# Optimization experiments

Measured on AMD Instinct MI355X. Metric: run time of the kernel, lower is better.

## Reference

```python
import jax, jax.numpy as jnp
import numpy as np

N = 100000
E = 1600000
IN_CH, HID_CH, OUT_CH, HEADS = 128, 32, 64, 4
NEG_SLOPE = 0.2


def gat_conv(x, src, dst, W, att_src, att_dst, bias, concat):
    """PyG-style GATConv (inference; dropout off). src/dst include self-loops.
    x: [N, Fin], W: [Fin, H*C], att_*: [H, C], bias: [H*C] or [C]."""
    n = x.shape[0]
    H, C = att_src.shape
    h = (x @ W).reshape(n, H, C)                      # [N, H, C]
    a_s = jnp.sum(h * att_src, axis=-1)               # [N, H]
    a_d = jnp.sum(h * att_dst, axis=-1)               # [N, H]
    e = jax.nn.leaky_relu(a_s[src] + a_d[dst], NEG_SLOPE)   # [E, H]
    # segment softmax over incoming edges of each dst node
    e_max = jax.ops.segment_max(e, dst, num_segments=n)     # [N, H]
    e_exp = jnp.exp(e - e_max[dst])                          # [E, H]
    denom = jax.ops.segment_sum(e_exp, dst, num_segments=n) # [N, H]
    alpha = e_exp / (denom[dst] + 1e-16)                     # [E, H]
    msg = h[src] * alpha[:, :, None]                         # [E, H, C]
    out = jax.ops.segment_sum(msg, dst, num_segments=n)     # [N, H, C]
    out = out.reshape(n, H * C) if concat else out.mean(axis=1)
    return out + bias


def setup_inputs() -> dict:
    key = jax.random.key(0)
    ks = jax.random.split(key, 10)
    g = 1.0 / np.sqrt(IN_CH)
    g2 = 1.0 / np.sqrt(HID_CH * HEADS)
    return {
        "x": jax.random.normal(ks[0], (N, IN_CH), dtype=jnp.float32),
        "edge_index": jax.random.randint(ks[1], (2, E), 0, N, dtype=jnp.int64),
        "W1": jax.random.normal(ks[2], (IN_CH, HEADS * HID_CH), dtype=jnp.float32) * g,
        "att_src1": jax.random.normal(ks[3], (HEADS, HID_CH), dtype=jnp.float32) * g,
        "att_dst1": jax.random.normal(ks[4], (HEADS, HID_CH), dtype=jnp.float32) * g,
        "b1": jnp.zeros((HEADS * HID_CH,), dtype=jnp.float32),
        "W2": jax.random.normal(ks[5], (HEADS * HID_CH, OUT_CH), dtype=jnp.float32) * g2,
        "att_src2": jax.random.normal(ks[6], (1, OUT_CH), dtype=jnp.float32) * g2,
        "att_dst2": jax.random.normal(ks[7], (1, OUT_CH), dtype=jnp.float32) * g2,
        "b2": jnp.zeros((OUT_CH,), dtype=jnp.float32),
    }


def reference(x, edge_index, W1, att_src1, att_dst1, b1, W2, att_src2, att_dst2, b2):
    n = x.shape[0]
    # GATConv adds self-loops by default (fixed-size concat: jit friendly)
    loops = jnp.arange(n, dtype=edge_index.dtype)
    src = jnp.concatenate([edge_index[0], loops])
    dst = jnp.concatenate([edge_index[1], loops])
    h = gat_conv(x, src, dst, W1, att_src1, att_dst1, b1, concat=True)
    h = jax.nn.elu(h)
    return gat_conv(h, src, dst, W2, att_src2, att_dst2, b2, concat=False)
```

## Files before the change

kernel.cpp:

```cpp
#include <hip/hip_runtime.h>
#include <hip/hip_fp16.h>

#define NEG_SLOPE 0.2f
#define BKN 128
#define MAXNB 1024
#define GRP 256
#define LOG2E 1.44269504f

typedef _Float16 half_t;
typedef __attribute__((ext_vector_type(2))) _Float16 half2v;
typedef __attribute__((ext_vector_type(4))) _Float16 half4;
typedef __attribute__((ext_vector_type(8))) _Float16 half8;
typedef __attribute__((ext_vector_type(4))) float floatx4;

#if __has_builtin(__builtin_amdgcn_fdot2)
#define FDOT2(a, b, c) __builtin_amdgcn_fdot2((a), (b), (c), false)
#else
#define FDOT2(a, b, c) ((float)(a)[0] * (float)(b)[0] + (float)(a)[1] * (float)(b)[1] + (c))
#endif

__global__ __launch_bounds__(256) void w_convert2(
    const float* __restrict__ W1, half_t* __restrict__ Wt1,
    const float* __restrict__ W2, half_t* __restrict__ Wt2)
{
    int i = blockIdx.x * 256 + threadIdx.x;
    if (i < 128 * 128) {
        int k = i / 128, nn = i % 128;
        Wt1[nn * 128 + k] = (half_t)W1[i];
    } else if (i < 128 * 128 + 128 * 64) {
        int j = i - 128 * 128;
        int k = j / 64, nn = j % 64;
        Wt2[nn * 128 + k] = (half_t)W2[j];
    }
}

template<int BN, int HEADS, bool INHALF>
__global__ __launch_bounds__(256) void gemm_mfma(
    const void* __restrict__ Xv, const half_t* __restrict__ Wt,
    const float* __restrict__ atts, const float* __restrict__ attd,
    half_t* __restrict__ H, float* __restrict__ As, float* __restrict__ Ad,
    int n)
{
    constexpr int K  = 128;
    constexpr int NT = BN / 16;
    constexpr int TPH = NT / HEADS;

    __shared__ half_t Wl[BN * K];
    __shared__ half_t Xl[64 * K];

    const int t = threadIdx.x;
    const int wave = t >> 6, lane = t & 63;
    const int quad = lane >> 4, c = lane & 15;

    float att_s[NT], att_d[NT];
    #pragma unroll
    for (int nt = 0; nt < NT; ++nt) {
        att_s[nt] = atts[nt * 16 + c] * LOG2E;
        att_d[nt] = attd[nt * 16 + c] * LOG2E;
    }

    for (int i = t; i < BN * 16; i += 256) {
        int row = i >> 4, cid = i & 15;
        half8 v = *(const half8*)(Wt + row * K + cid * 8);
        *(half8*)(Wl + row * K + ((cid ^ (row & 15)) << 3)) = v;
    }

    const int numTiles = (n + 63) / 64;
    for (int tile = blockIdx.x; tile < numTiles; tile += gridDim.x) {
        const int row0 = tile * 64;
        __syncthreads();
        for (int i = t; i < 1024; i += 256) {
            int m = i >> 4, cid = i & 15;
            int row = row0 + m;
            half8 h;
            #pragma unroll
            for (int z = 0; z < 8; ++z) h[z] = (half_t)0.f;
            if (row < n) {
                if constexpr (INHALF) {
                    h = *(const half8*)((const half_t*)Xv + (size_t)row * K + cid * 8);
                } else {
                    const float4* src = (const float4*)((const float*)Xv + (size_t)row * K + cid * 8);
                    float4 a = src[0], b = src[1];
                    h[0]=(half_t)a.x; h[1]=(half_t)a.y; h[2]=(half_t)a.z; h[3]=(half_t)a.w;
                    h[4]=(half_t)b.x; h[5]=(half_t)b.y; h[6]=(half_t)b.z; h[7]=(half_t)b.w;
                }
            }
            *(half8*)(Xl + m * K + ((cid ^ (m & 15)) << 3)) = h;
        }
        __syncthreads();

        floatx4 acc[NT];
        #pragma unroll
        for (int i = 0; i < NT; ++i) acc[i] = (floatx4)(0.f);

        #pragma unroll
        for (int kc = 0; kc < 4; ++kc) {
            int cid = kc * 4 + quad;
            half8 afrag = *(const half8*)(Xl + (wave * 16 + c) * K + ((cid ^ c) << 3));
            #pragma unroll
            for (int nt = 0; nt < NT; ++nt) {
                half8 bfrag = *(const half8*)(Wl + (nt * 16 + c) * K + ((cid ^ c) << 3));
                acc[nt] = __builtin_amdgcn_mfma_f32_16x16x32_f16(afrag, bfrag, acc[nt], 0, 0, 0);
            }
        }

        #pragma unroll
        for (int reg = 0; reg < 4; ++reg) {
            int row = row0 + wave * 16 + quad * 4 + reg;
            bool ok = row < n;
            if (ok) {
                #pragma unroll
                for (int nt = 0; nt < NT; ++nt)
                    H[(size_t)row * BN + nt * 16 + c] = (half_t)acc[nt][reg];
            }
            #pragma unroll
            for (int h = 0; h < HEADS; ++h) {
                float ps = 0.f, pd = 0.f;
                #pragma unroll
                for (int u = 0; u < TPH; ++u) {
                    int nt = h * TPH + u;
                    ps += acc[nt][reg] * att_s[nt];
                    pd += acc[nt][reg] * att_d[nt];
                }
                #pragma unroll
                for (int off = 1; off < 16; off <<= 1) {
                    ps += __shfl_xor(ps, off);
                    pd += __shfl_xor(pd, off);
                }
                if (ok && c == 0) {
                    As[(size_t)row * HEADS + h] = ps;
                    Ad[(size_t)row * HEADS + h] = pd;
                }
            }
        }
    }
}

__global__ __launch_bounds__(256) void ghist(
    const int* __restrict__ ei, int E, int Etot, int NB, int chunk,
    int* __restrict__ cnt)
{
    __shared__ int h[MAXNB];
    int g = blockIdx.x;
    for (int i = threadIdx.x; i < NB; i += 256) h[i] = 0;
    __syncthreads();
    int lo = g * chunk, hi = min(Etot, lo + chunk);
    for (int e = lo + threadIdx.x; e < hi; e += 256) {
        int dst = (e < E) ? ei[E + e] : (e - E);
        atomicAdd(&h[dst >> 7], 1);
    }
    __syncthreads();
    for (int i = threadIdx.x; i < NB; i += 256) cnt[i * GRP + g] = h[i];
}

__global__ __launch_bounds__(256) void scan_blocks(
    int* __restrict__ data, int n, int* __restrict__ bsum)
{
    __shared__ int s[256];
    int t = threadIdx.x;
    int idx = blockIdx.x * 1024 + t * 4;
    int4 v = make_int4(0, 0, 0, 0);
    if (idx + 3 < n)      v = *(const int4*)(data + idx);
    else {
        if (idx     < n) v.x = data[idx];
        if (idx + 1 < n) v.y = data[idx+1];
        if (idx + 2 < n) v.z = data[idx+2];
        if (idx + 3 < n) v.w = data[idx+3];
    }
    int tsum = v.x + v.y + v.z + v.w;
    s[t] = tsum;
    __syncthreads();
    for (int off = 1; off < 256; off <<= 1) {
        int x = (t >= off) ? s[t - off] : 0;
        __syncthreads();
        s[t] += x;
        __syncthreads();
    }
    int excl = s[t] - tsum;
    if (t == 255) bsum[blockIdx.x] = s[255];
    if (idx     < n) data[idx]     = excl;
    if (idx + 1 < n) data[idx + 1] = excl + v.x;
    if (idx + 2 < n) data[idx + 2] = excl + v.x + v.y;
    if (idx + 3 < n) data[idx + 3] = excl + v.x + v.y + v.z;
}

__global__ __launch_bounds__(256) void scan_sums(int* __restrict__ bsum, int nb)
{
    __shared__ int s[256];
    int t = threadIdx.x;
    int v = (t < nb) ? bsum[t] : 0;
    s[t] = v;
    __syncthreads();
    for (int off = 1; off < 256; off <<= 1) {
        int x = (t >= off) ? s[t - off] : 0;
        __syncthreads();
        s[t] += x;
        __syncthreads();
    }
    if (t < nb) bsum[t] = s[t] - v;
}

__global__ __launch_bounds__(256) void pass1_scatter(
    const int* __restrict__ ei, int E, int Etot, int NB, int chunk,
    const int* __restrict__ S, const int* __restrict__ bsum,
    unsigned* __restrict__ tmp)
{
    __shared__ int cur[MAXNB];
    int g = blockIdx.x;
    for (int i = threadIdx.x; i < NB; i += 256) {
        int idx = i * GRP + g;
        cur[i] = S[idx] + bsum[idx >> 10];
    }
    __syncthreads();
    int lo = g * chunk, hi = min(Etot, lo + chunk);
    for (int e = lo + threadIdx.x; e < hi; e += 256) {
        int src, dst;
        if (e < E) { src = ei[e]; dst = ei[E + e]; }
        else       { src = dst = e - E; }
        int pos = atomicAdd(&cur[dst >> 7], 1);
        tmp[pos] = ((unsigned)src << 7) | (unsigned)(dst & (BKN - 1));
    }
}

__global__ __launch_bounds__(256) void pass2_sort(
    const unsigned* __restrict__ tmp, const int* __restrict__ S,
    const int* __restrict__ bsum, int NB, int Etot,
    int* __restrict__ offs, int* __restrict__ esrc, int n)
{
    __shared__ int cnt[BKN];
    __shared__ int sc[BKN];
    __shared__ int cur[BKN];
    int bk = blockIdx.x;
    int t  = threadIdx.x;
    if (t < BKN) cnt[t] = 0;
    __syncthreads();
    int lo = S[bk * GRP] + bsum[(bk * GRP) >> 10];
    int hi = (bk + 1 < NB) ? (S[(bk + 1) * GRP] + bsum[((bk + 1) * GRP) >> 10]) : Etot;
    for (int i = lo + t; i < hi; i += 256)
        atomicAdd(&cnt[tmp[i] & (BKN - 1)], 1);
    __syncthreads();
    int v = (t < BKN) ? cnt[t] : 0;
    if (t < BKN) sc[t] = v;
    __syncthreads();
    for (int off = 1; off < BKN; off <<= 1) {
        int x = (t < BKN && t >= off) ? sc[t - off] : 0;
        __syncthreads();
        if (t < BKN) sc[t] += x;
        __syncthreads();
    }
    if (t < BKN) {
        int node = bk * BKN + t;
        if (node < n) offs[node] = lo + sc[t];
        cur[t] = lo + sc[t] - v;
    }
    __syncthreads();
    for (int i = lo + t; i < hi; i += 256) {
        unsigned w = tmp[i];
        int p = atomicAdd(&cur[w & (BKN - 1)], 1);
        esrc[p] = (int)(w >> 7);
    }
}

__global__ __launch_bounds__(256) void agg1(
    const int* __restrict__ offs, const int* __restrict__ esrc,
    const half8* __restrict__ H8, const float* __restrict__ As,
    const float* __restrict__ Ad, const float* __restrict__ bias,
    half_t* __restrict__ X2h, int n)
{
    int v    = (blockIdx.x * 256 + threadIdx.x) >> 6;
    int lane = threadIdx.x & 63;
    if (v >= n) return;
    int q    = lane >> 4;
    int li   = lane & 15;
    int head = li >> 2;
    int end = offs[v];
    int beg = v ? offs[v - 1] : 0;
    float adv = Ad[(size_t)v * 4 + head];
    half2v one; one[0] = (half_t)1.f; one[1] = (half_t)1.f;
    float a[8];
    #pragma unroll
    for (int f = 0; f < 8; ++f) a[f] = 0.f;
    float den = 0.f;
    int j = beg + q;
    for (; j + 12 < end; j += 16) {
        int s0 = esrc[j], s1 = esrc[j + 4], s2 = esrc[j + 8], s3 = esrc[j + 12];
        float e0 = As[(unsigned)(s0 * 4 + head)] + adv;
        float e1 = As[(unsigned)(s1 * 4 + head)] + adv;
        float e2 = As[(unsigned)(s2 * 4 + head)] + adv;
        float e3 = As[(unsigned)(s3 * 4 + head)] + adv;
        half8 q0 = H8[(unsigned)(s0 * 16 + li)];
        half8 q1 = H8[(unsigned)(s1 * 16 + li)];
        half8 q2 = H8[(unsigned)(s2 * 16 + li)];
        half8 q3 = H8[(unsigned)(s3 * 16 + li)];
        float w0 = __builtin_amdgcn_exp2f(fmaxf(e0, NEG_SLOPE * e0));
        float w1 = __builtin_amdgcn_exp2f(fmaxf(e1, NEG_SLOPE * e1));
        float w2 = __builtin_amdgcn_exp2f(fmaxf(e2, NEG_SLOPE * e2));
        float w3 = __builtin_amdgcn_exp2f(fmaxf(e3, NEG_SLOPE * e3));
        half2v wp01; wp01[0] = (half_t)w0; wp01[1] = (half_t)w1;
        half2v wp23; wp23[0] = (half_t)w2; wp23[1] = (half_t)w3;
        #pragma unroll
        for (int f = 0; f < 8; ++f) {
            half2v p01; p01[0] = q0[f]; p01[1] = q1[f];
            half2v p23; p23[0] = q2[f]; p23[1] = q3[f];
            a[f] = FDOT2(p01, wp01, a[f]);
            a[f] = FDOT2(p23, wp23, a[f]);
        }
        den = FDOT2(wp01, one, den);
        den = FDOT2(wp23, one, den);
    }
    for (; j + 4 < end; j += 8) {
        int s0 = esrc[j], s1 = esrc[j + 4];
        float e0 = As[(unsigned)(s0 * 4 + head)] + adv;
        float e1 = As[(unsigned)(s1 * 4 + head)] + adv;
        half8 q0 = H8[(unsigned)(s0 * 16 + li)];
        half8 q1 = H8[(unsigned)(s1 * 16 + li)];
        float w0 = __builtin_amdgcn_exp2f(fmaxf(e0, NEG_SLOPE * e0));
        float w1 = __builtin_amdgcn_exp2f(fmaxf(e1, NEG_SLOPE * e1));
        half2v wp; wp[0] = (half_t)w0; wp[1] = (half_t)w1;
        #pragma unroll
        for (int f = 0; f < 8; ++f) {
            half2v p; p[0] = q0[f]; p[1] = q1[f];
            a[f] = FDOT2(p, wp, a[f]);
        }
        den = FDOT2(wp, one, den);
    }
    for (; j < end; j += 4) {
        int s = esrc[j];
        float e = As[(unsigned)(s * 4 + head)] + adv;
        half8 q0 = H8[(unsigned)(s * 16 + li)];
        float w = __builtin_amdgcn_exp2f(fmaxf(e, NEG_SLOPE * e));
        #pragma unroll
        for (int f = 0; f < 8; ++f) a[f] += w * (float)q0[f];
        den += w;
    }
    #pragma unroll
    for (int f = 0; f < 8; ++f) {
        a[f] += __shfl_xor(a[f], 16);
        a[f] += __shfl_xor(a[f], 32);
    }
    den += __shfl_xor(den, 16);
    den += __shfl_xor(den, 32);
    if (q == 0) {
        float inv = 1.f / (den + 1e-16f);
        float4 b0 = ((const float4*)bias)[2 * li];
        float4 b1 = ((const float4*)bias)[2 * li + 1];
        float o[8];
        o[0] = a[0] * inv + b0.x; o[1] = a[1] * inv + b0.y;
        o[2] = a[2] * inv + b0.z; o[3] = a[3] * inv + b0.w;
        o[4] = a[4] * inv + b1.x; o[5] = a[5] * inv + b1.y;
        o[6] = a[6] * inv + b1.z; o[7] = a[7] * inv + b1.w;
        half8 h;
        #pragma unroll
        for (int f = 0; f < 8; ++f) {
            float e = o[f] > 0.f ? o[f] : __expf(o[f]) - 1.f;
            h[f] = (half_t)e;
        }
        *(half8*)(X2h + (size_t)v * 128 + li * 8) = h;
    }
}

__global__ __launch_bounds__(256) void agg2(
    const int* __restrict__ offs, const int* __restrict__ esrc,
    const half8* __restrict__ H8, const float* __restrict__ As,
    const float* __restrict__ Ad, const float* __restrict__ bias,
    float* __restrict__ out, int n)
{
    int v    = (blockIdx.x * 256 + threadIdx.x) >> 6;
    int lane = threadIdx.x & 63;
    if (v >= n) return;
    int g  = lane >> 3;
    int li = lane & 7;
    int end = offs[v];
    int beg = v ? offs[v - 1] : 0;
    float adv = Ad[v];
    half2v one; one[0] = (half_t)1.f; one[1] = (half_t)1.f;
    float a[8];
    #pragma unroll
    for (int f = 0; f < 8; ++f) a[f] = 0.f;
    float den = 0.f;
    int j = beg + g;
    for (; j + 24 < end; j += 32) {
        int s0 = esrc[j], s1 = esrc[j + 8], s2 = esrc[j + 16], s3 = esrc[j + 24];
        float e0 = As[s0] + adv;
        float e1 = As[s1] + adv;
        float e2 = As[s2] + adv;
        float e3 = As[s3] + adv;
        half8 q0 = H8[(unsigned)(s0 * 8 + li)];
        half8 q1 = H8[(unsigned)(s1 * 8 + li)];
        half8 q2 = H8[(unsigned)(s2 * 8 + li)];
        half8 q3 = H8[(unsigned)(s3 * 8 + li)];
        float w0 = __builtin_amdgcn_exp2f(fmaxf(e0, NEG_SLOPE * e0));
        float w1 = __builtin_amdgcn_exp2f(fmaxf(e1, NEG_SLOPE * e1));
        float w2 = __builtin_amdgcn_exp2f(fmaxf(e2, NEG_SLOPE * e2));
        float w3 = __builtin_amdgcn_exp2f(fmaxf(e3, NEG_SLOPE * e3));
        half2v wp01; wp01[0] = (half_t)w0; wp01[1] = (half_t)w1;
        half2v wp23; wp23[0] = (half_t)w2; wp23[1] = (half_t)w3;
        #pragma unroll
        for (int f = 0; f < 8; ++f) {
            half2v p01; p01[0] = q0[f]; p01[1] = q1[f];
            half2v p23; p23[0] = q2[f]; p23[1] = q3[f];
            a[f] = FDOT2(p01, wp01, a[f]);
            a[f] = FDOT2(p23, wp23, a[f]);
        }
        den = FDOT2(wp01, one, den);
        den = FDOT2(wp23, one, den);
    }
    for (; j + 8 < end; j += 16) {
        int s0 = esrc[j], s1 = esrc[j + 8];
        float e0 = As[s0] + adv;
        float e1 = As[s1] + adv;
        half8 q0 = H8[(unsigned)(s0 * 8 + li)];
        half8 q1 = H8[(unsigned)(s1 * 8 + li)];
        float w0 = __builtin_amdgcn_exp2f(fmaxf(e0, NEG_SLOPE * e0));
        float w1 = __builtin_amdgcn_exp2f(fmaxf(e1, NEG_SLOPE * e1));
        half2v wp; wp[0] = (half_t)w0; wp[1] = (half_t)w1;
        #pragma unroll
        for (int f = 0; f < 8; ++f) {
            half2v p; p[0] = q0[f]; p[1] = q1[f];
            a[f] = FDOT2(p, wp, a[f]);
        }
        den = FDOT2(wp, one, den);
    }
    for (; j < end; j += 8) {
        int s = esrc[j];
        float e = As[s] + adv;
        half8 q0 = H8[(unsigned)(s * 8 + li)];
        float w = __builtin_amdgcn_exp2f(fmaxf(e, NEG_SLOPE * e));
        #pragma unroll
        for (int f = 0; f < 8; ++f) a[f] += w * (float)q0[f];
        den += w;
    }
    #pragma unroll
    for (int f = 0; f < 8; ++f) {
        a[f] += __shfl_xor(a[f], 8);
        a[f] += __shfl_xor(a[f], 16);
        a[f] += __shfl_xor(a[f], 32);
    }
    den += __shfl_xor(den, 8);
    den += __shfl_xor(den, 16);
    den += __shfl_xor(den, 32);
    if (lane < 8) {
        float inv = 1.f / (den + 1e-16f);
        float4 b0 = ((const float4*)bias)[2 * li];
        float4 b1 = ((const float4*)bias)[2 * li + 1];
        float4* o4 = (float4*)(out + (size_t)v * 64);
        o4[2 * li]     = make_float4(a[0] * inv + b0.x, a[1] * inv + b0.y,
                                     a[2] * inv + b0.z, a[3] * inv + b0.w);
        o4[2 * li + 1] = make_float4(a[4] * inv + b1.x, a[5] * inv + b1.y,
                                     a[6] * inv + b1.z, a[7] * inv + b1.w);
    }
}

extern "C" void kernel_launch(void* const* d_in, const int* in_sizes, int n_in,
                              void* d_out, int out_size, void* d_ws, size_t ws_size,
                              hipStream_t stream)
{
    (void)n_in; (void)out_size; (void)ws_size;
    const float* x   = (const float*)d_in[0];
    const int*   ei  = (const int*)  d_in[1];
    const float* W1  = (const float*)d_in[2];
    const float* as1 = (const float*)d_in[3];
    const float* ad1 = (const float*)d_in[4];
    const float* b1  = (const float*)d_in[5];
    const float* W2  = (const float*)d_in[6];
    const float* as2 = (const float*)d_in[7];
    const float* ad2 = (const float*)d_in[8];
    const float* b2  = (const float*)d_in[9];
    float* out = (float*)d_out;

    const int n    = in_sizes[0] / 128;
    const int E    = in_sizes[1] / 2;
    const int Etot = E + n;
    const int NB   = (n + BKN - 1) / BKN;
    const int chunk = (Etot + GRP - 1) / GRP;

    char* p = (char*)d_ws;
    half_t* Hh  = (half_t*)p; p += (size_t)n * 128 * sizeof(half_t);
    half_t* X2h = (half_t*)p; p += (size_t)n * 128 * sizeof(half_t);
    float* As1 = (float*)p;   p += (size_t)n * 4 * sizeof(float);
    float* Ad1 = (float*)p;   p += (size_t)n * 4 * sizeof(float);
    int* offs  = (int*)p;     p += (size_t)n * sizeof(int);
    int* esrc  = (int*)p;     p += (size_t)Etot * sizeof(int);
    unsigned* tmp = (unsigned*)p; p += (size_t)Etot * sizeof(unsigned);
    int* cnt   = (int*)p;     p += (size_t)NB * GRP * sizeof(int);
    int* bsum  = (int*)p;     p += 1024;
    half_t* Wt1 = (half_t*)p; p += 128 * 128 * sizeof(half_t);
    half_t* Wt2 = (half_t*)p; p += 64 * 128 * sizeof(half_t);

    const int scan_n  = NB * GRP;
    const int scan_nb = (scan_n + 1023) / 1024;

    w_convert2<<<(128 * 192 + 255) / 256, 256, 0, stream>>>(W1, Wt1, W2, Wt2);

    ghist<<<GRP, 256, 0, stream>>>(ei, E, Etot, NB, chunk, cnt);
    scan_blocks<<<scan_nb, 256, 0, stream>>>(cnt, scan_n, bsum);
    scan_sums<<<1, 256, 0, stream>>>(bsum, scan_nb);
    pass1_scatter<<<GRP, 256, 0, stream>>>(ei, E, Etot, NB, chunk, cnt, bsum, tmp);
    pass2_sort<<<NB, 256, 0, stream>>>(tmp, cnt, bsum, NB, Etot, offs, esrc, n);

    const int gtiles = (n + 63) / 64;

    gemm_mfma<128, 4, false><<<gtiles, 256, 0, stream>>>(x, Wt1, as1, ad1, Hh, As1, Ad1, n);
    agg1<<<(n * 64 + 255) / 256, 256, 0, stream>>>(offs, esrc, (const half8*)Hh, As1, Ad1, b1, X2h, n);

    gemm_mfma<64, 1, true><<<gtiles, 256, 0, stream>>>(X2h, Wt2, as2, ad2, Hh, As1, Ad1, n);
    agg2<<<(n * 64 + 255) / 256, 256, 0, stream>>>(offs, esrc, (const half8*)Hh, As1, Ad1, b2, out, n);
}
```

Before: 320.7 us.

## Replace two-pass bucket sort CSR build with per-node atomic counting sort

Replaces the bucketed histogram, scatter and per-bucket local sort with a per-node degree histogram using global atomics, a scan over node degrees, and a single scatter pass that writes source indices directly through per-node atomic cursors. Weight conversion is folded into the histogram kernel, and block sums are added lazily in the aggregation kernels. This removes one full pass over the edges and the temporary packed buffer, at the cost of contended global atomics and non-deterministic edge order within each node.

```diff
diff --git a/kernel.cpp b/kernel.cpp
--- a/kernel.cpp
+++ b/kernel.cpp
@@ -2,9 +2,6 @@
 #include <hip/hip_fp16.h>
 
 #define NEG_SLOPE 0.2f
-#define BKN 128
-#define MAXNB 1024
-#define GRP 256
 #define LOG2E 1.44269504f
 
 typedef _Float16 half_t;
@@ -18,21 +15,6 @@
 #else
 #define FDOT2(a, b, c) ((float)(a)[0] * (float)(b)[0] + (float)(a)[1] * (float)(b)[1] + (c))
 #endif
-
-__global__ __launch_bounds__(256) void w_convert2(
-    const float* __restrict__ W1, half_t* __restrict__ Wt1,
-    const float* __restrict__ W2, half_t* __restrict__ Wt2)
-{
-    int i = blockIdx.x * 256 + threadIdx.x;
-    if (i < 128 * 128) {
-        int k = i / 128, nn = i % 128;
-        Wt1[nn * 128 + k] = (half_t)W1[i];
-    } else if (i < 128 * 128 + 128 * 64) {
-        int j = i - 128 * 128;
-        int k = j / 64, nn = j % 64;
-        Wt2[nn * 128 + k] = (half_t)W2[j];
-    }
-}
 
 template<int BN, int HEADS, bool INHALF>
 __global__ __launch_bounds__(256) void gemm_mfma(
@@ -136,36 +118,41 @@
     }
 }
 
-__global__ __launch_bounds__(256) void ghist(
-    const int* __restrict__ ei, int E, int Etot, int NB, int chunk,
-    int* __restrict__ cnt)
-{
-    __shared__ int h[MAXNB];
-    int g = blockIdx.x;
-    for (int i = threadIdx.x; i < NB; i += 256) h[i] = 0;
-    __syncthreads();
-    int lo = g * chunk, hi = min(Etot, lo + chunk);
-    for (int e = lo + threadIdx.x; e < hi; e += 256) {
+__global__ __launch_bounds__(256) void ghist_g(
+    const int* __restrict__ ei, int E, int Etot, int* __restrict__ deg,
+    const float* __restrict__ W1, half_t* __restrict__ Wt1,
+    const float* __restrict__ W2, half_t* __restrict__ Wt2)
+{
+    int iw = blockIdx.x * 256 + threadIdx.x;
+    if (iw < 128 * 128) {
+        int k = iw / 128, nn = iw % 128;
+        Wt1[nn * 128 + k] = (half_t)W1[iw];
+    } else if (iw < 128 * 128 + 128 * 64) {
+        int jx = iw - 128 * 128;
+        int k = jx / 64, nn = jx % 64;
+        Wt2[nn * 128 + k] = (half_t)W2[jx];
+    }
+    int stride = gridDim.x * 256;
+    for (int e = blockIdx.x * 256 + threadIdx.x; e < Etot; e += stride) {
         int dst = (e < E) ? ei[E + e] : (e - E);
-        atomicAdd(&h[dst >> 7], 1);
-    }
-    __syncthreads();
-    for (int i = threadIdx.x; i < NB; i += 256) cnt[i * GRP + g] = h[i];
-}
-
-__global__ __launch_bounds__(256) void scan_blocks(
-    int* __restrict__ data, int n, int* __restrict__ bsum)
+        atomicAdd(&deg[dst], 1);
+    }
+}
+
+__global__ __launch_bounds__(256) void scan_blocks_dc(
+    const int* __restrict__ deg, int n, int* __restrict__ offs,
+    int* __restrict__ cur, int* __restrict__ bsum)
 {
     __shared__ int s[256];
     int t = threadIdx.x;
     int idx = blockIdx.x * 1024 + t * 4;
     int4 v = make_int4(0, 0, 0, 0);
-    if (idx + 3 < n)      v = *(const int4*)(data + idx);
+    if (idx + 3 < n)      v = *(const int4*)(deg + idx);
     else {
-        if (idx     < n) v.x = data[idx];
-        if (idx + 1 < n) v.y = data[idx+1];
-        if (idx + 2 < n) v.z = data[idx+2];
-        if (idx + 3 < n) v.w = data[idx+3];
+        if (idx     < n) v.x = deg[idx];
+        if (idx + 1 < n) v.y = deg[idx+1];
+        if (idx + 2 < n) v.z = deg[idx+2];
+        if (idx + 3 < n) v.w = deg[idx+3];
     }
     int tsum = v.x + v.y + v.z + v.w;
     s[t] = tsum;
@@ -178,10 +165,11 @@
     }
     int excl = s[t] - tsum;
     if (t == 255) bsum[blockIdx.x] = s[255];
-    if (idx     < n) data[idx]     = excl;
-    if (idx + 1 < n) data[idx + 1] = excl + v.x;
-    if (idx + 2 < n) data[idx + 2] = excl + v.x + v.y;
-    if (idx + 3 < n) data[idx + 3] = excl + v.x + v.y + v.z;
+    int p0 = excl, p1 = p0 + v.x, p2 = p1 + v.y, p3 = p2 + v.z;
+    if (idx     < n) { cur[idx]     = p0; offs[idx]     = p1; }
+    if (idx + 1 < n) { cur[idx + 1] = p1; offs[idx + 1] = p2; }
+    if (idx + 2 < n) { cur[idx + 2] = p2; offs[idx + 2] = p3; }
+    if (idx + 3 < n) { cur[idx + 3] = p3; offs[idx + 3] = p3 + v.w; }
 }
 
 __global__ __launch_bounds__(256) void scan_sums(int* __restrict__ bsum, int nb)
@@ -200,69 +188,24 @@
     if (t < nb) bsum[t] = s[t] - v;
 }
 
-__global__ __launch_bounds__(256) void pass1_scatter(
-    const int* __restrict__ ei, int E, int Etot, int NB, int chunk,
-    const int* __restrict__ S, const int* __restrict__ bsum,
-    unsigned* __restrict__ tmp)
-{
-    __shared__ int cur[MAXNB];
-    int g = blockIdx.x;
-    for (int i = threadIdx.x; i < NB; i += 256) {
-        int idx = i * GRP + g;
-        cur[i] = S[idx] + bsum[idx >> 10];
-    }
-    __syncthreads();
-    int lo = g * chunk, hi = min(Etot, lo + chunk);
-    for (int e = lo + threadIdx.x; e < hi; e += 256) {
+__global__ __launch_bounds__(256) void pass_scatter_g(
+    const int* __restrict__ ei, int E, int Etot,
+    int* __restrict__ cur, const int* __restrict__ bsum,
+    int* __restrict__ esrc)
+{
+    int stride = gridDim.x * 256;
+    for (int e = blockIdx.x * 256 + threadIdx.x; e < Etot; e += stride) {
         int src, dst;
         if (e < E) { src = ei[e]; dst = ei[E + e]; }
         else       { src = dst = e - E; }
-        int pos = atomicAdd(&cur[dst >> 7], 1);
-        tmp[pos] = ((unsigned)src << 7) | (unsigned)(dst & (BKN - 1));
-    }
-}
-
-__global__ __launch_bounds__(256) void pass2_sort(
-    const unsigned* __restrict__ tmp, const int* __restrict__ S,
-    const int* __restrict__ bsum, int NB, int Etot,
-    int* __restrict__ offs, int* __restrict__ esrc, int n)
-{
-    __shared__ int cnt[BKN];
-    __shared__ int sc[BKN];
-    __shared__ int cur[BKN];
-    int bk = blockIdx.x;
-    int t  = threadIdx.x;
-    if (t < BKN) cnt[t] = 0;
-    __syncthreads();
-    int lo = S[bk * GRP] + bsum[(bk * GRP) >> 10];
-    int hi = (bk + 1 < NB) ? (S[(bk + 1) * GRP] + bsum[((bk + 1) * GRP) >> 10]) : Etot;
-    for (int i = lo + t; i < hi; i += 256)
-        atomicAdd(&cnt[tmp[i] & (BKN - 1)], 1);
-    __syncthreads();
-    int v = (t < BKN) ? cnt[t] : 0;
-    if (t < BKN) sc[t] = v;
-    __syncthreads();
-    for (int off = 1; off < BKN; off <<= 1) {
-        int x = (t < BKN && t >= off) ? sc[t - off] : 0;
-        __syncthreads();
-        if (t < BKN) sc[t] += x;
-        __syncthreads();
-    }
-    if (t < BKN) {
-        int node = bk * BKN + t;
-        if (node < n) offs[node] = lo + sc[t];
-        cur[t] = lo + sc[t] - v;
-    }
-    __syncthreads();
-    for (int i = lo + t; i < hi; i += 256) {
-        unsigned w = tmp[i];
-        int p = atomicAdd(&cur[w & (BKN - 1)], 1);
-        esrc[p] = (int)(w >> 7);
+        int pos = atomicAdd(&cur[dst], 1) + bsum[dst >> 10];
+        esrc[pos] = src;
     }
 }
 
 __global__ __launch_bounds__(256) void agg1(
-    const int* __restrict__ offs, const int* __restrict__ esrc,
+    const int* __restrict__ offs, const int* __restrict__ bsum,
+    const int* __restrict__ esrc,
     const half8* __restrict__ H8, const float* __restrict__ As,
     const float* __restrict__ Ad, const float* __restrict__ bias,
     half_t* __restrict__ X2h, int n)
@@ -273,8 +216,8 @@
     int q    = lane >> 4;
     int li   = lane & 15;
     int head = li >> 2;
-    int end = offs[v];
-    int beg = v ? offs[v - 1] : 0;
+    int end = offs[v] + bsum[v >> 10];
+    int beg = v ? (offs[v - 1] + bsum[(v - 1) >> 10]) : 0;
     float adv = Ad[(size_t)v * 4 + head];
     half2v one; one[0] = (half_t)1.f; one[1] = (half_t)1.f;
     float a[8];
@@ -360,7 +303,8 @@
 }
 
 __global__ __launch_bounds__(256) void agg2(
-    const int* __restrict__ offs, const int* __restrict__ esrc,
+    const int* __restrict__ offs, const int* __restrict__ bsum,
+    const int* __restrict__ esrc,
     const half8* __restrict__ H8, const float* __restrict__ As,
     const float* __restrict__ Ad, const float* __restrict__ bias,
     float* __restrict__ out, int n)
@@ -370,8 +314,8 @@
     if (v >= n) return;
     int g  = lane >> 3;
     int li = lane & 7;
-    int end = offs[v];
-    int beg = v ? offs[v - 1] : 0;
+    int end = offs[v] + bsum[v >> 10];
+    int beg = v ? (offs[v - 1] + bsum[(v - 1) >> 10]) : 0;
     float adv = Ad[v];
     half2v one; one[0] = (half_t)1.f; one[1] = (half_t)1.f;
     float a[8];
@@ -471,38 +415,33 @@
     const int n    = in_sizes[0] / 128;
     const int E    = in_sizes[1] / 2;
     const int Etot = E + n;
-    const int NB   = (n + BKN - 1) / BKN;
-    const int chunk = (Etot + GRP - 1) / GRP;
 
     char* p = (char*)d_ws;
     half_t* Hh  = (half_t*)p; p += (size_t)n * 128 * sizeof(half_t);
     half_t* X2h = (half_t*)p; p += (size_t)n * 128 * sizeof(half_t);
     float* As1 = (float*)p;   p += (size_t)n * 4 * sizeof(float);
     float* Ad1 = (float*)p;   p += (size_t)n * 4 * sizeof(float);
+    int* deg   = (int*)p;     p += (size_t)n * sizeof(int);
     int* offs  = (int*)p;     p += (size_t)n * sizeof(int);
+    int* cur   = (int*)p;     p += (size_t)n * sizeof(int);
     int* esrc  = (int*)p;     p += (size_t)Etot * sizeof(int);
-    unsigned* tmp = (unsigned*)p; p += (size_t)Etot * sizeof(unsigned);
-    int* cnt   = (int*)p;     p += (size_t)NB * GRP * sizeof(int);
     int* bsum  = (int*)p;     p += 1024;
     half_t* Wt1 = (half_t*)p; p += 128 * 128 * sizeof(half_t);
     half_t* Wt2 = (half_t*)p; p += 64 * 128 * sizeof(half_t);
 
-    const int scan_n  = NB * GRP;
-    const int scan_nb = (scan_n + 1023) / 1024;
-
-    w_convert2<<<(128 * 192 + 255) / 256, 256, 0, stream>>>(W1, Wt1, W2, Wt2);
-
-    ghist<<<GRP, 256, 0, stream>>>(ei, E, Etot, NB, chunk, cnt);
-    scan_blocks<<<scan_nb, 256, 0, stream>>>(cnt, scan_n, bsum);
+    const int scan_nb = (n + 1023) / 1024;
+
+    hipMemsetAsync(deg, 0, (size_t)n * sizeof(int), stream);
+    ghist_g<<<1024, 256, 0, stream>>>(ei, E, Etot, deg, W1, Wt1, W2, Wt2);
+    scan_blocks_dc<<<scan_nb, 256, 0, stream>>>(deg, n, offs, cur, bsum);
     scan_sums<<<1, 256, 0, stream>>>(bsum, scan_nb);
-    pass1_scatter<<<GRP, 256, 0, stream>>>(ei, E, Etot, NB, chunk, cnt, bsum, tmp);
-    pass2_sort<<<NB, 256, 0, stream>>>(tmp, cnt, bsum, NB, Etot, offs, esrc, n);
+    pass_scatter_g<<<1024, 256, 0, stream>>>(ei, E, Etot, cur, bsum, esrc);
 
     const int gtiles = (n + 63) / 64;
 
     gemm_mfma<128, 4, false><<<gtiles, 256, 0, stream>>>(x, Wt1, as1, ad1, Hh, As1, Ad1, n);
-    agg1<<<(n * 64 + 255) / 256, 256, 0, stream>>>(offs, esrc, (const half8*)Hh, As1, Ad1, b1, X2h, n);
+    agg1<<<(n * 64 + 255) / 256, 256, 0, stream>>>(offs, bsum, esrc, (const half8*)Hh, As1, Ad1, b1, X2h, n);
 
     gemm_mfma<64, 1, true><<<gtiles, 256, 0, stream>>>(X2h, Wt2, as2, ad2, Hh, As1, Ad1, n);
-    agg2<<<(n * 64 + 255) / 256, 256, 0, stream>>>(offs, esrc, (const half8*)Hh, As1, Ad1, b2, out, n);
-}
+    agg2<<<(n * 64 + 255) / 256, 256, 0, stream>>>(offs, bsum, esrc, (const half8*)Hh, As1, Ad1, b2, out, n);
+}
```

Result: slower. 461.1 us (+43.8%).

## Fuse weight conversion into histogram and overlap layer-1 GEMM with edge scatter

Applied to the files above, without the earlier changes.

Folds the weight fp16 transpose into the histogram kernel and merges the edge scatter pass with the first MFMA GEMM into one heterogeneous launch. The first GRP blocks do the scatter and the rest process GEMM tiles. This cuts two kernel launches and lets the compute-heavy GEMM overlap the atomic-bound scatter. In exchange, the shared memory footprint grows for all blocks, and the scatter and GEMM blocks compete for CUs.

```diff
diff --git a/kernel.cpp b/kernel.cpp
--- a/kernel.cpp
+++ b/kernel.cpp
@@ -18,21 +18,6 @@
 #else
 #define FDOT2(a, b, c) ((float)(a)[0] * (float)(b)[0] + (float)(a)[1] * (float)(b)[1] + (c))
 #endif
-
-__global__ __launch_bounds__(256) void w_convert2(
-    const float* __restrict__ W1, half_t* __restrict__ Wt1,
-    const float* __restrict__ W2, half_t* __restrict__ Wt2)
-{
-    int i = blockIdx.x * 256 + threadIdx.x;
-    if (i < 128 * 128) {
-        int k = i / 128, nn = i % 128;
-        Wt1[nn * 128 + k] = (half_t)W1[i];
-    } else if (i < 128 * 128 + 128 * 64) {
-        int j = i - 128 * 128;
-        int k = j / 64, nn = j % 64;
-        Wt2[nn * 128 + k] = (half_t)W2[j];
-    }
-}
 
 template<int BN, int HEADS, bool INHALF>
 __global__ __launch_bounds__(256) void gemm_mfma(
@@ -136,10 +121,22 @@
     }
 }
 
-__global__ __launch_bounds__(256) void ghist(
+__global__ __launch_bounds__(256) void ghist_wconv(
     const int* __restrict__ ei, int E, int Etot, int NB, int chunk,
-    int* __restrict__ cnt)
-{
+    int* __restrict__ cnt,
+    const float* __restrict__ W1, half_t* __restrict__ Wt1,
+    const float* __restrict__ W2, half_t* __restrict__ Wt2)
+{
+    int iw = blockIdx.x * 256 + threadIdx.x;
+    if (iw < 128 * 128) {
+        int k = iw / 128, nn = iw % 128;
+        Wt1[nn * 128 + k] = (half_t)W1[iw];
+    } else if (iw < 128 * 128 + 128 * 64) {
+        int jx = iw - 128 * 128;
+        int k = jx / 64, nn = jx % 64;
+        Wt2[nn * 128 + k] = (half_t)W2[jx];
+    }
+
     __shared__ int h[MAXNB];
     int g = blockIdx.x;
     for (int i = threadIdx.x; i < NB; i += 256) h[i] = 0;
@@ -200,25 +197,120 @@
     if (t < nb) bsum[t] = s[t] - v;
 }
 
-__global__ __launch_bounds__(256) void pass1_scatter(
+__global__ __launch_bounds__(256) void pass1_gemm1(
     const int* __restrict__ ei, int E, int Etot, int NB, int chunk,
     const int* __restrict__ S, const int* __restrict__ bsum,
-    unsigned* __restrict__ tmp)
-{
+    unsigned* __restrict__ tmp,
+    const float* __restrict__ X, const half_t* __restrict__ Wt,
+    const float* __restrict__ atts, const float* __restrict__ attd,
+    half_t* __restrict__ H, float* __restrict__ As, float* __restrict__ Ad,
+    int n)
+{
+    constexpr int K = 128, BN = 128, NT = 8, HEADS = 4, TPH = 2;
+    __shared__ half_t Wl[BN * K];
+    __shared__ half_t Xl[64 * K];
     __shared__ int cur[MAXNB];
-    int g = blockIdx.x;
-    for (int i = threadIdx.x; i < NB; i += 256) {
-        int idx = i * GRP + g;
-        cur[i] = S[idx] + bsum[idx >> 10];
-    }
-    __syncthreads();
-    int lo = g * chunk, hi = min(Etot, lo + chunk);
-    for (int e = lo + threadIdx.x; e < hi; e += 256) {
-        int src, dst;
-        if (e < E) { src = ei[e]; dst = ei[E + e]; }
-        else       { src = dst = e - E; }
-        int pos = atomicAdd(&cur[dst >> 7], 1);
-        tmp[pos] = ((unsigned)src << 7) | (unsigned)(dst & (BKN - 1));
+
+    const int t = threadIdx.x;
+
+    if (blockIdx.x < GRP) {
+        int g = blockIdx.x;
+        for (int i = t; i < NB; i += 256) {
+            int idx = i * GRP + g;
+            cur[i] = S[idx] + bsum[idx >> 10];
+        }
+        __syncthreads();
+        int lo = g * chunk, hi = min(Etot, lo + chunk);
+        for (int e = lo + t; e < hi; e += 256) {
+            int src, dst;
+            if (e < E) { src = ei[e]; dst = ei[E + e]; }
+            else       { src = dst = e - E; }
+            int pos = atomicAdd(&cur[dst >> 7], 1);
+            tmp[pos] = ((unsigned)src << 7) | (unsigned)(dst & (BKN - 1));
+        }
+        return;
+    }
+
+    const int wave = t >> 6, lane = t & 63;
+    const int quad = lane >> 4, c = lane & 15;
+
+    float att_s[NT], att_d[NT];
+    #pragma unroll
+    for (int nt = 0; nt < NT; ++nt) {
+        att_s[nt] = atts[nt * 16 + c] * LOG2E;
+        att_d[nt] = attd[nt * 16 + c] * LOG2E;
+    }
+
+    for (int i = t; i < BN * 16; i += 256) {
+        int row = i >> 4, cid = i & 15;
+        half8 v = *(const half8*)(Wt + row * K + cid * 8);
+        *(half8*)(Wl + row * K + ((cid ^ (row & 15)) << 3)) = v;
+    }
+
+    const int numTiles = (n + 63) / 64;
+    for (int tile = blockIdx.x - GRP; tile < numTiles; tile += gridDim.x - GRP) {
+        const int row0 = tile * 64;
+        __syncthreads();
+        for (int i = t; i < 1024; i += 256) {
+            int m = i >> 4, cid = i & 15;
+            int row = row0 + m;
+            half8 h;
+            #pragma unroll
+            for (int z = 0; z < 8; ++z) h[z] = (half_t)0.f;
+            if (row < n) {
+                const float4* src = (const float4*)(X + (size_t)row * K + cid * 8);
+                float4 a = src[0], b = src[1];
+                h[0]=(half_t)a.x; h[1]=(half_t)a.y; h[2]=(half_t)a.z; h[3]=(half_t)a.w;
+                h[4]=(half_t)b.x; h[5]=(half_t)b.y; h[6]=(half_t)b.z; h[7]=(half_t)b.w;
+            }
+            *(half8*)(Xl + m * K + ((cid ^ (m & 15)) << 3)) = h;
+        }
+        __syncthreads();
+
+        floatx4 acc[NT];
+        #pragma unroll
+        for (int i = 0; i < NT; ++i) acc[i] = (floatx4)(0.f);
+
+        #pragma unroll
+        for (int kc = 0; kc < 4; ++kc) {
+            int cid = kc * 4 + quad;
+            half8 afrag = *(const half8*)(Xl + (wave * 16 + c) * K + ((cid ^ c) << 3));
+            #pragma unroll
+            for (int nt = 0; nt < NT; ++nt) {
+                half8 bfrag = *(const half8*)(Wl + (nt * 16 + c) * K + ((cid ^ c) << 3));
+                acc[nt] = __builtin_amdgcn_mfma_f32_16x16x32_f16(afrag, bfrag, acc[nt], 0, 0, 0);
+            }
+        }
+
+        #pragma unroll
+        for (int reg = 0; reg < 4; ++reg) {
+            int row = row0 + wave * 16 + quad * 4 + reg;
+            bool ok = row < n;
+            if (ok) {
+                #pragma unroll
+                for (int nt = 0; nt < NT; ++nt)
+                    H[(size_t)row * BN + nt * 16 + c] = (half_t)acc[nt][reg];
+            }
+            #pragma unroll
+            for (int h = 0; h < HEADS; ++h) {
+                float ps = 0.f, pd = 0.f;
+                #pragma unroll
+                for (int u = 0; u < TPH; ++u) {
+                    int nt = h * TPH + u;
+                    ps += acc[nt][reg] * att_s[nt];
+                    pd += acc[nt][reg] * att_d[nt];
+                }
+                #pragma unroll
+                for (int off = 1; off < 16; off <<= 1) {
+                    ps += __shfl_xor(ps, off);
+                    pd += __shfl_xor(pd, off);
+                }
+                if (ok && c == 0) {
+                    As[(size_t)row * HEADS + h] = ps;
+                    Ad[(size_t)row * HEADS + h] = pd;
+                }
+            }
+        }
     }
 }
 
@@ -490,17 +582,15 @@
     const int scan_n  = NB * GRP;
     const int scan_nb = (scan_n + 1023) / 1024;
 
-    w_convert2<<<(128 * 192 + 255) / 256, 256, 0, stream>>>(W1, Wt1, W2, Wt2);
-
-    ghist<<<GRP, 256, 0, stream>>>(ei, E, Etot, NB, chunk, cnt);
+    const int gtiles = (n + 63) / 64;
+
+    ghist_wconv<<<GRP, 256, 0, stream>>>(ei, E, Etot, NB, chunk, cnt, W1, Wt1, W2, Wt2);
     scan_blocks<<<scan_nb, 256, 0, stream>>>(cnt, scan_n, bsum);
     scan_sums<<<1, 256, 0, stream>>>(bsum, scan_nb);
-    pass1_scatter<<<GRP, 256, 0, stream>>>(ei, E, Etot, NB, chunk, cnt, bsum, tmp);
+    pass1_gemm1<<<GRP + gtiles, 256, 0, stream>>>(ei, E, Etot, NB, chunk, cnt, bsum, tmp,
+                                                  x, Wt1, as1, ad1, Hh, As1, Ad1, n);
     pass2_sort<<<NB, 256, 0, stream>>>(tmp, cnt, bsum, NB, Etot, offs, esrc, n);
 
-    const int gtiles = (n + 63) / 64;
-
-    gemm_mfma<128, 4, false><<<gtiles, 256, 0, stream>>>(x, Wt1, as1, ad1, Hh, As1, Ad1, n);
     agg1<<<(n * 64 + 255) / 256, 256, 0, stream>>>(offs, esrc, (const half8*)Hh, As1, Ad1, b1, X2h, n);
 
     gemm_mfma<64, 1, true><<<gtiles, 256, 0, stream>>>(X2h, Wt2, as2, ad2, Hh, As1, Ad1, n);
```

Result: faster. 305.0 us (-4.9%).
